# Optimization experiments

Measured on AMD Instinct MI355X. Metric: run time of the kernel, lower is better.

Reference implementation:

```python
import jax, jax.numpy as jnp
import numpy as np

NUM_GRAPHS = 256  # static batch size (= batch_indices.max()+1 by construction)
EMBED = 32
HIDDEN = 256
DEPTH = 10


def setup_inputs() -> dict:
    key = jax.random.key(0)
    ks = jax.random.split(key, 16)
    N, M = 8192, 16384
    atom_features = jax.random.randint(ks[0], (N,), 0, 200, dtype=jnp.int32)
    bond_features = jax.random.randint(ks[1], (M,), 0, 10, dtype=jnp.int32)
    adjacency_matrix = jax.random.randint(ks[2], (N, N), 0, 2, dtype=jnp.int32)
    batch_indices = jnp.sort(jax.random.randint(ks[3], (N,), 0, NUM_GRAPHS, dtype=jnp.int32))
    s = 0.05
    atom_emb_table = jax.random.normal(ks[4], (200, EMBED), jnp.float32) * s
    bond_emb_table = jax.random.normal(ks[5], (10, EMBED), jnp.float32) * s
    msg_W = jax.random.normal(ks[6], (DEPTH, HIDDEN, 2 * EMBED), jnp.float32) * s
    msg_b = jax.random.normal(ks[7], (DEPTH, HIDDEN), jnp.float32) * s
    gru_Wih = jax.random.normal(ks[8], (DEPTH, 3 * EMBED, HIDDEN), jnp.float32) * s
    gru_Whh = jax.random.normal(ks[9], (DEPTH, 3 * EMBED, EMBED), jnp.float32) * s
    gru_bih = jax.random.normal(ks[10], (DEPTH, 3 * EMBED), jnp.float32) * s
    gru_bhh = jax.random.normal(ks[11], (DEPTH, 3 * EMBED), jnp.float32) * s
    pool_W = jax.random.normal(ks[12], (HIDDEN, EMBED), jnp.float32) * s
    pool_b = jax.random.normal(ks[13], (HIDDEN,), jnp.float32) * s
    return dict(atom_features=atom_features, bond_features=bond_features,
                adjacency_matrix=adjacency_matrix, batch_indices=batch_indices,
                atom_emb_table=atom_emb_table, bond_emb_table=bond_emb_table,
                msg_W=msg_W, msg_b=msg_b, gru_Wih=gru_Wih, gru_Whh=gru_Whh,
                gru_bih=gru_bih, gru_bhh=gru_bhh, pool_W=pool_W, pool_b=pool_b)


def _gru_step(x, h, Wih, Whh, bih, bhh):
    # single-step torch-style GRU cell: x [N,HIDDEN], h [N,EMBED]
    gi = x @ Wih.T + bih                      # [N, 3E]
    gh = h @ Whh.T + bhh                      # [N, 3E]
    i_r, i_z, i_n = jnp.split(gi, 3, axis=-1)
    h_r, h_z, h_n = jnp.split(gh, 3, axis=-1)
    r = jax.nn.sigmoid(i_r + h_r)
    z = jax.nn.sigmoid(i_z + h_z)
    n = jnp.tanh(i_n + r * h_n)
    return (1.0 - z) * n + z * h


def reference(atom_features, bond_features, adjacency_matrix, batch_indices,
              atom_emb_table, bond_emb_table, msg_W, msg_b,
              gru_Wih, gru_Whh, gru_bih, gru_bhh, pool_W, pool_b):
    h = atom_emb_table[atom_features]                      # [N, E]
    A = (adjacency_matrix != 0).astype(h.dtype)            # [N, N]
    deg = A.sum(axis=-1, keepdims=True)                    # [N, 1]
    inv_deg = 1.0 / jnp.maximum(deg, 1.0)
    has_nei = deg > 0
    for d in range(DEPTH):
        # mean over neighbors of Linear(concat(self, nei)) == affine in (self, mean_nei)
        nei_mean = (A @ h) * inv_deg                       # [N, E]
        W_self = msg_W[d][:, :EMBED]                       # [H, E]
        W_nei = msg_W[d][:, EMBED:]                        # [H, E]
        msg = h @ W_self.T + nei_mean @ W_nei.T + msg_b[d]  # [N, H]
        msg = jnp.where(has_nei, msg, 0.0)                 # zero message if no neighbors
        h = _gru_step(msg, h, gru_Wih[d], gru_Whh[d], gru_bih[d], gru_bhh[d])
        # dropout is identity in eval mode
    # segment-mean pooling over graphs (zeros for empty graphs)
    sums = jax.ops.segment_sum(h, batch_indices, num_segments=NUM_GRAPHS)      # [B, E]
    counts = jax.ops.segment_sum(jnp.ones((h.shape[0],), h.dtype), batch_indices,
                                 num_segments=NUM_GRAPHS)[:, None]             # [B, 1]
    graph_mean = jnp.where(counts > 0, sums / jnp.maximum(counts, 1.0), 0.0)
    graph_embeddings = graph_mean @ pool_W.T + pool_b                          # [B, H]
    bond_embeddings = bond_emb_table[bond_features]                            # [M, E]
    return h, bond_embeddings, graph_embeddings
```

## Files before the change

### kernel.cpp

```cpp
#include <hip/hip_runtime.h>
#include <stdint.h>

#define N_ATOMS 8192
#define EMBED   32
#define DEPTHN  10

typedef short bf16x8 __attribute__((ext_vector_type(8)));
typedef float f32x4  __attribute__((ext_vector_type(4)));

__device__ __forceinline__ unsigned short f2bf(float f){
    unsigned u = __builtin_bit_cast(unsigned, f);
    u = u + 0x7FFFu + ((u >> 16) & 1u);
    return (unsigned short)(u >> 16);
}

__global__ __launch_bounds__(256) void k_preA(const int* __restrict__ A,
                                              unsigned long long* __restrict__ mask,
                                              int row0)
{
    const int i = row0 + blockIdx.x;
    const int t = threadIdx.x, w = t >> 6, l = t & 63;
    const int* row = A + (size_t)i * N_ATOMS;
    __shared__ unsigned long long lm[128];
    #pragma unroll
    for (int k = 0; k < 32; ++k){
        int j = k*256 + t;
        unsigned long long m = __ballot(row[j] != 0);
        if (l == 0) lm[k*4 + w] = m;
    }
    __syncthreads();
    if (t < 128) mask[(size_t)i*128 + t] = lm[t];
}

__global__ __launch_bounds__(256) void k_pre2(
    const int* __restrict__ A, unsigned* __restrict__ mP,
    float* __restrict__ deg, float* __restrict__ invdeg,
    const int* __restrict__ af, const float* __restrict__ atom_emb,
    const float* __restrict__ msgW, const float* __restrict__ msgb,
    const float* __restrict__ Wih, const float* __restrict__ bih,
    float* __restrict__ hA, unsigned short* __restrict__ hP,
    float* __restrict__ Wc, float* __restrict__ bc,
    const int* __restrict__ bfeat, const float* __restrict__ bondf,
    float* __restrict__ out1)
{
    const int t = threadIdx.x;
    __shared__ unsigned lm[256];
    __shared__ int red[4];
    if (blockIdx.x < 8192){
        const int blk = blockIdx.x;
        const int grp = (blk >> 7)*8 + (blk & 7);
        const int n   = (blk >> 3) & 15;
        const int i   = grp*16 + n;
        const int w = t >> 6, l = t & 63;
        const int* row = A + (size_t)i * N_ATOMS;
        #pragma unroll
        for (int k = 0; k < 32; ++k){
            int j = k*256 + t;
            unsigned long long m = __ballot(row[j] != 0);
            if (l == 0){
                lm[(k*4 + w)*2]     = (unsigned)m;
                lm[(k*4 + w)*2 + 1] = (unsigned)(m >> 32);
            }
        }
        __syncthreads();
        int cnt = __popc(lm[t]);
        #pragma unroll
        for (int off = 32; off >= 1; off >>= 1) cnt += __shfl_down(cnt, off, 64);
        if (l == 0) red[w] = cnt;
        __syncthreads();
        if (t == 0){
            int s = red[0] + red[1] + red[2] + red[3];
            deg[i] = (float)s;
            invdeg[i] = 1.f / fmaxf((float)s, 1.f);
        }
        mP[(size_t)grp*4096 + t*16 + n] = lm[t];
    } else {
        const int blk = blockIdx.x - 8192;
        if (blk < 1024){
            int idx = blk*256 + t;
            int i = idx >> 5, e = idx & 31;
            float v = atom_emb[af[i]*EMBED + e];
            hA[idx] = v;
            int g = i >> 5, qd = (i >> 3) & 3, j8 = i & 7;
            hP[(size_t)((g*2 + (e>>4))*64 + qd*16 + (e&15))*8 + j8] = f2bf(v);
        } else if (blk < 1264){
            int o = (blk-1024)*256 + t;
            int d = o / 6144, r = o % 6144, g = r >> 6, e = r & 63;
            const float* wi = Wih  + (size_t)(d*96 + g)*256;
            const float* mw = msgW + (size_t)d*256*64 + e;
            float acc = 0.f;
            for (int hh = 0; hh < 256; ++hh) acc += wi[hh] * mw[hh*64];
            Wc[o] = acc;
        } else if (blk < 1268){
            int o = (blk-1264)*256 + t;
            if (o < 960){
                int d = o / 96;
                const float* wi = Wih + (size_t)o*256;
                const float* mb = msgb + d*256;
                float acc = 0.f;
                for (int hh = 0; hh < 256; ++hh) acc += wi[hh] * mb[hh];
                bc[o] = acc + bih[o];
            }
        } else {
            int idx = (blk-1268)*256 + t;
            out1[idx] = bondf[bfeat[idx >> 5]*EMBED + (idx & 31)];
        }
    }
}

__global__ __launch_bounds__(256) void k_prep(
    const unsigned* __restrict__ maskRM, unsigned* __restrict__ mP,
    float* __restrict__ deg, float* __restrict__ invdeg,
    const int* __restrict__ af, const float* __restrict__ atom_emb,
    const float* __restrict__ msgW, const float* __restrict__ msgb,
    const float* __restrict__ Wih, const float* __restrict__ bih,
    float* __restrict__ hA, unsigned short* __restrict__ hP,
    float* __restrict__ Wc, float* __restrict__ bc,
    const int* __restrict__ bfeat, const float* __restrict__ bondf,
    float* __restrict__ out1)
{
    const int t = threadIdx.x;
    if (blockIdx.x < 512){
        const int grp = blockIdx.x;
        __shared__ unsigned lm[16*260];
        __shared__ int red[256];
        #pragma unroll
        for (int s = 0; s < 16; ++s)
            lm[s*260 + t] = maskRM[(size_t)grp*4096 + s*256 + t];
        __syncthreads();
        {
            int r = t >> 4, seg = t & 15, cnt = 0;
            #pragma unroll
            for (int k = 0; k < 16; ++k) cnt += __popc(lm[r*260 + seg*16 + k]);
            red[t] = cnt; __syncthreads();
            if (t < 16){
                int s = 0;
                #pragma unroll
                for (int k = 0; k < 16; ++k) s += red[t*16 + k];
                deg[grp*16 + t] = (float)s;
                invdeg[grp*16 + t] = 1.f / fmaxf((float)s, 1.f);
            }
        }
        unsigned* out = mP + (size_t)grp*4096;
        #pragma unroll
        for (int s = 0; s < 16; ++s){
            int W = s*256 + t;
            out[W] = lm[(W & 15)*260 + (W >> 4)];
        }
    } else {
        const int blk = blockIdx.x - 512;
        if (blk < 1024){
            int idx = blk*256 + t;
            int i = idx >> 5, e = idx & 31;
            float v = atom_emb[af[i]*EMBED + e];
            hA[idx] = v;
            int g = i >> 5, qd = (i >> 3) & 3, j8 = i & 7;
            hP[(size_t)((g*2 + (e>>4))*64 + qd*16 + (e&15))*8 + j8] = f2bf(v);
        } else if (blk < 1264){
            int o = (blk-1024)*256 + t;
            int d = o / 6144, r = o % 6144, g = r >> 6, e = r & 63;
            const float* wi = Wih  + (size_t)(d*96 + g)*256;
            const float* mw = msgW + (size_t)d*256*64 + e;
            float acc = 0.f;
            for (int hh = 0; hh < 256; ++hh) acc += wi[hh] * mw[hh*64];
            Wc[o] = acc;
        } else if (blk < 1268){
            int o = (blk-1264)*256 + t;
            if (o < 960){
                int d = o / 96;
                const float* wi = Wih + (size_t)o*256;
                const float* mb = msgb + d*256;
                float acc = 0.f;
                for (int hh = 0; hh < 256; ++hh) acc += wi[hh] * mb[hh];
                bc[o] = acc + bih[o];
            }
        } else {
            int idx = (blk-1268)*256 + t;
            out1[idx] = bondf[bfeat[idx >> 5]*EMBED + (idx & 31)];
        }
    }
}

__global__ __launch_bounds__(512) void k_depth(
    const unsigned short* __restrict__ hPin,
    const unsigned* __restrict__ mP,
    const float* __restrict__ hin, float* __restrict__ hout,
    const float* __restrict__ invdeg, const float* __restrict__ deg,
    const float* __restrict__ Wc, const float* __restrict__ bc,
    const float* __restrict__ bihf, const float* __restrict__ bhhf,
    const float* __restrict__ Whhf,
    unsigned short* __restrict__ hPout, float* __restrict__ out0, int last)
{
    __shared__ uint2 lut[16];
    __shared__ float part[8][32][33];
    __shared__ float xs[32][68];
    const int t = threadIdx.x, blk = blockIdx.x;
    if (t < 16){
        unsigned lo = ((t & 1) ? 0x3F80u : 0u) | ((t & 2) ? 0x3F800000u : 0u);
        unsigned hi = ((t & 4) ? 0x3F80u : 0u) | ((t & 8) ? 0x3F800000u : 0u);
        lut[t] = make_uint2(lo, hi);
    }
    __syncthreads();
    {
        const int q = t >> 6, lane = t & 63;
        const int n = lane & 15, quad = lane >> 4;
        const int rt0 = blk*2;
        f32x4 a00 = {0.f,0.f,0.f,0.f};
        f32x4 a01 = {0.f,0.f,0.f,0.f};
        f32x4 a10 = {0.f,0.f,0.f,0.f};
        f32x4 a11 = {0.f,0.f,0.f,0.f};
        const unsigned* m0 = mP + (size_t)rt0*4096 + n;
        const unsigned* m1 = m0 + 4096;
        #pragma unroll 4
        for (int kk = 0; kk < 32; ++kk){
            const int g = q*32 + kk;
            union { uint4 u; bf16x8 v; } b0, b1;
            b0.u = *(const uint4*)&hPin[(size_t)((g*2+0)*64 + lane)*8];
            b1.u = *(const uint4*)&hPin[(size_t)((g*2+1)*64 + lane)*8];
            unsigned by0 = (m0[g*16] >> (quad*8)) & 0xFFu;
            unsigned by1 = (m1[g*16] >> (quad*8)) & 0xFFu;
            union { uint2 dd[2]; bf16x8 v; } af0, af1;
            af0.dd[0] = lut[by0 & 15u];
            af0.dd[1] = lut[by0 >> 4];
            af1.dd[0] = lut[by1 & 15u];
            af1.dd[1] = lut[by1 >> 4];
            a00 = __builtin_amdgcn_mfma_f32_16x16x32_bf16(af0.v, b0.v, a00, 0, 0, 0);
            a01 = __builtin_amdgcn_mfma_f32_16x16x32_bf16(af0.v, b1.v, a01, 0, 0, 0);
            a10 = __builtin_amdgcn_mfma_f32_16x16x32_bf16(af1.v, b0.v, a10, 0, 0, 0);
            a11 = __builtin_amdgcn_mfma_f32_16x16x32_bf16(af1.v, b1.v, a11, 0, 0, 0);
        }
        #pragma unroll
        for (int r = 0; r < 4; ++r){
            int rl = quad*4 + r;
            part[q][rl][n]       = a00[r];
            part[q][rl][16+n]    = a01[r];
            part[q][16+rl][n]    = a10[r];
            part[q][16+rl][16+n] = a11[r];
        }
    }
    __syncthreads();
    {
        #pragma unroll
        for (int ii = 0; ii < 2; ++ii){
            int i = ii*512 + t;
            int a = i >> 5, e = i & 31;
            float s = 0.f;
            #pragma unroll
            for (int q = 0; q < 8; ++q) s += part[q][a][e];
            xs[a][32+e] = s;
            xs[a][e] = hin[(size_t)blk*1024 + i];
        }
    }
    __syncthreads();
    {
        const int a = t & 15, pw = t >> 4;
        const int al = a + (pw & 16);
        const int p  = pw & 15;
        const int atom = blk*32 + al;
        const float idg = invdeg[atom];
        const bool nz = deg[atom] > 0.f;
        float x[64];
        #pragma unroll
        for (int r = 0; r < 16; ++r){
            float4 v = *(const float4*)&xs[al][r*4];
            x[r*4+0]=v.x; x[r*4+1]=v.y; x[r*4+2]=v.z; x[r*4+3]=v.w;
        }
        #pragma unroll
        for (int e = 32; e < 64; ++e) x[e] *= idg;
        const int gg = atom >> 5, qd = (atom >> 3) & 3, j8 = atom & 7;
        #pragma unroll
        for (int jj = 0; jj < 2; ++jj){
            const int j = p*2 + jj;
            const float* wr = Wc + j*64;
            const float* wz = Wc + (32+j)*64;
            const float* wn = Wc + (64+j)*64;
            float gr=0.f, gz=0.f, gn=0.f;
            #pragma unroll
            for (int e = 0; e < 64; ++e){ gr += wr[e]*x[e]; gz += wz[e]*x[e]; gn += wn[e]*x[e]; }
            if (nz){ gr += bc[j]; gz += bc[32+j]; gn += bc[64+j]; }
            else   { gr  = bihf[j]; gz = bihf[32+j]; gn = bihf[64+j]; }
            const float* vr = Whhf + j*32;
            const float* vz = Whhf + (32+j)*32;
            const float* vn = Whhf + (64+j)*32;
            float hr=bhhf[j], hz=bhhf[32+j], hn=bhhf[64+j];
            #pragma unroll
            for (int e = 0; e < 32; ++e){ hr += vr[e]*x[e]; hz += vz[e]*x[e]; hn += vn[e]*x[e]; }
            float rg = 1.f/(1.f + expf(-(gr+hr)));
            float zg = 1.f/(1.f + expf(-(gz+hz)));
            float ng = tanhf(gn + rg*hn);
            float hnew = (1.f - zg)*ng + zg*x[j];
            hout[(size_t)atom*EMBED + j] = hnew;
            hPout[(size_t)((gg*2 + (j>>4))*64 + qd*16 + (j&15))*8 + j8] = f2bf(hnew);
            if (last) out0[(size_t)atom*EMBED + j] = hnew;
        }
    }
}

__global__ __launch_bounds__(256) void k_pool(
    const float* __restrict__ h, const int* __restrict__ batch,
    const float* __restrict__ poolW, const float* __restrict__ poolb,
    float* __restrict__ out2)
{
    const int b = blockIdx.x, t = threadIdx.x;
    int lo, hi;
    { int l = 0, r = N_ATOMS; while (l < r){ int m = (l+r)>>1; if (batch[m] < b)   l = m+1; else r = m; } lo = l; }
    { int l = 0, r = N_ATOMS; while (l < r){ int m = (l+r)>>1; if (batch[m] < b+1) l = m+1; else r = m; } hi = l; }
    const int cnt = hi - lo;
    __shared__ float ps[8][32];
    __shared__ float mean[32];
    const int e = t & 31, g = t >> 5;
    float acc = 0.f;
    for (int a = lo + g; a < hi; a += 8) acc += h[(size_t)a*EMBED + e];
    ps[g][e] = acc; __syncthreads();
    if (t < 32){
        float s = 0.f;
        #pragma unroll
        for (int gg = 0; gg < 8; ++gg) s += ps[gg][t];
        mean[t] = (cnt > 0) ? s / (float)cnt : 0.f;
    }
    __syncthreads();
    float emb = poolb[t];
    #pragma unroll
    for (int ee = 0; ee < 32; ++ee) emb += mean[ee] * poolW[t*32 + ee];
    out2[b*256 + t] = emb;
}

extern "C" void kernel_launch(void* const* d_in, const int* in_sizes, int n_in,
                              void* d_out, int out_size, void* d_ws, size_t ws_size,
                              hipStream_t stream)
{
    (void)in_sizes; (void)n_in; (void)out_size;
    const int* af   = (const int*)d_in[0];
    const int* bfe  = (const int*)d_in[1];
    const int* A    = (const int*)d_in[2];
    const int* bidx = (const int*)d_in[3];
    const float* atom_emb = (const float*)d_in[4];
    const float* bond_emb = (const float*)d_in[5];
    const float* msgW  = (const float*)d_in[6];
    const float* msgb  = (const float*)d_in[7];
    const float* Wih   = (const float*)d_in[8];
    const float* Whh   = (const float*)d_in[9];
    const float* bih   = (const float*)d_in[10];
    const float* bhh   = (const float*)d_in[11];
    const float* poolW = (const float*)d_in[12];
    const float* poolb = (const float*)d_in[13];

    float* out0 = (float*)d_out;
    float* out1 = out0 + 262144;
    float* out2 = out1 + 524288;

    float* deg    = out2;
    float* invdeg = out2 + 8192;

    unsigned*       mP;
    float*          hA; float* hB; float* Wc; float* bc;
    unsigned short* hP0; unsigned short* hP1;
    const int wsok = (ws_size >= (size_t)33554432) ? 1 : 0;
    if (wsok){
        char* W = (char*)d_ws;
        mP      = (unsigned*)(W + 8388608);
        hP0     = (unsigned short*)(W + 16777216);
        hA      = (float*)(W + 17825792);
        hB      = (float*)(W + 18874368);
        Wc      = (float*)(W + 19922944);
        bc      = (float*)(W + 20185088);
        hP1     = (unsigned short*)(W + 20971520);
        k_pre2<<<dim3(11508), dim3(256), 0, stream>>>(A, mP, deg, invdeg,
            af, atom_emb, msgW, msgb, Wih, bih, hA, hP0, Wc, bc,
            bfe, bond_emb, out1);
    } else {
        unsigned long long* maskRM;
        char* Ab = (char*)d_in[2];
        hA      = (float*)(Ab + 0);
        hB      = (float*)(Ab + 1048576);
        hP0     = (unsigned short*)(Ab + 2097152);
        Wc      = (float*)(Ab + 2621440);
        bc      = (float*)(Ab + 2867200);
        hP1     = (unsigned short*)(Ab + 4194304);
        mP      = (unsigned*)(Ab + 13631488);
        maskRM  = (unsigned long long*)(Ab + 260046848);
        k_preA<<<dim3(1),    dim3(256), 0, stream>>>(A, maskRM, 8191);
        k_preA<<<dim3(7),    dim3(256), 0, stream>>>(A, maskRM, 8184);
        k_preA<<<dim3(248),  dim3(256), 0, stream>>>(A, maskRM, 7936);
        k_preA<<<dim3(7936), dim3(256), 0, stream>>>(A, maskRM, 0);
        k_prep<<<dim3(3828), dim3(256), 0, stream>>>((const unsigned*)maskRM, mP,
            deg, invdeg, af, atom_emb, msgW, msgb, Wih, bih, hA, hP0, Wc, bc,
            bfe, bond_emb, out1);
    }

    float* hin = hA; float* hout = hB;
    unsigned short* hPi = hP0; unsigned short* hPo = hP1;
    for (int d = 0; d < DEPTHN; ++d){
        k_depth<<<dim3(256), dim3(512), 0, stream>>>(hPi, mP, hin, hout,
            invdeg, deg, Wc + d*6144, bc + d*96, bih + d*96, bhh + d*96,
            Whh + d*3072, hPo, out0, (d == DEPTHN-1) ? 1 : 0);
        float* tf = hin; hin = hout; hout = tf;
        unsigned short* tp = hPi; hPi = hPo; hPo = tp;
    }
    k_pool<<<dim3(256), dim3(256), 0, stream>>>(hin, bidx, poolW, poolb, out2);
}
```

Baseline: 666.5 us.

## Process 64 atoms per depth block to reuse h tiles across four row tiles

Each k_depth block now covers 64 atoms (four 16-row mask tiles) instead of 32, so every loaded bf16 h fragment feeds eight MFMAs rather than four. This halves global reads of h per depth step. The partial-sum reduction now runs in two phases through a smaller shared buffer to fit LDS, and the GRU stage gives each thread four output columns. The grid shrinks to 128 blocks, which lowers parallelism on a GPU with many CUs, and k_pre2 block ordering is swapped so the mask-packing blocks come after the other preprocessing blocks.

Measured after the change: 800.6 us. +20.1%, slower.

```diff
diff --git a/kernel.cpp b/kernel.cpp
--- a/kernel.cpp
+++ b/kernel.cpp
@@ -46,8 +46,8 @@
     const int t = threadIdx.x;
     __shared__ unsigned lm[256];
     __shared__ int red[4];
-    if (blockIdx.x < 8192){
-        const int blk = blockIdx.x;
+    if (blockIdx.x >= 3316){
+        const int blk = blockIdx.x - 3316;
         const int grp = (blk >> 7)*8 + (blk & 7);
         const int n   = (blk >> 3) & 15;
         const int i   = grp*16 + n;
@@ -75,7 +75,7 @@
         }
         mP[(size_t)grp*4096 + t*16 + n] = lm[t];
     } else {
-        const int blk = blockIdx.x - 8192;
+        const int blk = blockIdx.x;
         if (blk < 1024){
             int idx = blk*256 + t;
             int i = idx >> 5, e = idx & 31;
@@ -192,8 +192,8 @@
     unsigned short* __restrict__ hPout, float* __restrict__ out0, int last)
 {
     __shared__ uint2 lut[16];
-    __shared__ float part[8][32][33];
-    __shared__ float xs[32][68];
+    __shared__ float part[4][64][33];
+    __shared__ float xs[64][68];
     const int t = threadIdx.x, blk = blockIdx.x;
     if (t < 16){
         unsigned lo = ((t & 1) ? 0x3F80u : 0u) | ((t & 2) ? 0x3F800000u : 0u);
@@ -201,62 +201,77 @@
         lut[t] = make_uint2(lo, hi);
     }
     __syncthreads();
+    const int q = t >> 6, lane = t & 63;
+    const int n = lane & 15, quad = lane >> 4;
     {
-        const int q = t >> 6, lane = t & 63;
-        const int n = lane & 15, quad = lane >> 4;
-        const int rt0 = blk*2;
-        f32x4 a00 = {0.f,0.f,0.f,0.f};
-        f32x4 a01 = {0.f,0.f,0.f,0.f};
-        f32x4 a10 = {0.f,0.f,0.f,0.f};
-        f32x4 a11 = {0.f,0.f,0.f,0.f};
-        const unsigned* m0 = mP + (size_t)rt0*4096 + n;
-        const unsigned* m1 = m0 + 4096;
+        const int rt0 = blk*4;
+        f32x4 acc[4][2];
+        #pragma unroll
+        for (int r = 0; r < 4; ++r){
+            acc[r][0] = (f32x4){0.f,0.f,0.f,0.f};
+            acc[r][1] = (f32x4){0.f,0.f,0.f,0.f};
+        }
+        const unsigned* mb_ = mP + (size_t)rt0*4096 + n;
         #pragma unroll 4
         for (int kk = 0; kk < 32; ++kk){
             const int g = q*32 + kk;
             union { uint4 u; bf16x8 v; } b0, b1;
             b0.u = *(const uint4*)&hPin[(size_t)((g*2+0)*64 + lane)*8];
             b1.u = *(const uint4*)&hPin[(size_t)((g*2+1)*64 + lane)*8];
-            unsigned by0 = (m0[g*16] >> (quad*8)) & 0xFFu;
-            unsigned by1 = (m1[g*16] >> (quad*8)) & 0xFFu;
-            union { uint2 dd[2]; bf16x8 v; } af0, af1;
-            af0.dd[0] = lut[by0 & 15u];
-            af0.dd[1] = lut[by0 >> 4];
-            af1.dd[0] = lut[by1 & 15u];
-            af1.dd[1] = lut[by1 >> 4];
-            a00 = __builtin_amdgcn_mfma_f32_16x16x32_bf16(af0.v, b0.v, a00, 0, 0, 0);
-            a01 = __builtin_amdgcn_mfma_f32_16x16x32_bf16(af0.v, b1.v, a01, 0, 0, 0);
-            a10 = __builtin_amdgcn_mfma_f32_16x16x32_bf16(af1.v, b0.v, a10, 0, 0, 0);
-            a11 = __builtin_amdgcn_mfma_f32_16x16x32_bf16(af1.v, b1.v, a11, 0, 0, 0);
-        }
-        #pragma unroll
-        for (int r = 0; r < 4; ++r){
-            int rl = quad*4 + r;
-            part[q][rl][n]       = a00[r];
-            part[q][rl][16+n]    = a01[r];
-            part[q][16+rl][n]    = a10[r];
-            part[q][16+rl][16+n] = a11[r];
+            #pragma unroll
+            for (int rt = 0; rt < 4; ++rt){
+                unsigned by = (mb_[(size_t)rt*4096 + g*16] >> (quad*8)) & 0xFFu;
+                union { uint2 dd[2]; bf16x8 v; } afx;
+                afx.dd[0] = lut[by & 15u];
+                afx.dd[1] = lut[by >> 4];
+                acc[rt][0] = __builtin_amdgcn_mfma_f32_16x16x32_bf16(afx.v, b0.v, acc[rt][0], 0, 0, 0);
+                acc[rt][1] = __builtin_amdgcn_mfma_f32_16x16x32_bf16(afx.v, b1.v, acc[rt][1], 0, 0, 0);
+            }
+        }
+        if (q < 4){
+            #pragma unroll
+            for (int rt = 0; rt < 4; ++rt)
+                #pragma unroll
+                for (int r = 0; r < 4; ++r){
+                    int rl = rt*16 + quad*4 + r;
+                    part[q][rl][n]      = acc[rt][0][r];
+                    part[q][rl][16+n]   = acc[rt][1][r];
+                }
+        }
+        __syncthreads();
+        float s[4];
+        #pragma unroll
+        for (int k = 0; k < 4; ++k){
+            int i = k*512 + t;
+            int a2 = i >> 5, e = i & 31;
+            s[k] = part[0][a2][e] + part[1][a2][e] + part[2][a2][e] + part[3][a2][e];
+            xs[a2][e] = hin[(size_t)blk*2048 + i];
+        }
+        __syncthreads();
+        if (q >= 4){
+            #pragma unroll
+            for (int rt = 0; rt < 4; ++rt)
+                #pragma unroll
+                for (int r = 0; r < 4; ++r){
+                    int rl = rt*16 + quad*4 + r;
+                    part[q-4][rl][n]    = acc[rt][0][r];
+                    part[q-4][rl][16+n] = acc[rt][1][r];
+                }
+        }
+        __syncthreads();
+        #pragma unroll
+        for (int k = 0; k < 4; ++k){
+            int i = k*512 + t;
+            int a2 = i >> 5, e = i & 31;
+            s[k] += part[0][a2][e] + part[1][a2][e] + part[2][a2][e] + part[3][a2][e];
+            xs[a2][32+e] = s[k];
         }
     }
     __syncthreads();
     {
-        #pragma unroll
-        for (int ii = 0; ii < 2; ++ii){
-            int i = ii*512 + t;
-            int a = i >> 5, e = i & 31;
-            float s = 0.f;
-            #pragma unroll
-            for (int q = 0; q < 8; ++q) s += part[q][a][e];
-            xs[a][32+e] = s;
-            xs[a][e] = hin[(size_t)blk*1024 + i];
-        }
-    }
-    __syncthreads();
-    {
-        const int a = t & 15, pw = t >> 4;
-        const int al = a + (pw & 16);
-        const int p  = pw & 15;
-        const int atom = blk*32 + al;
+        const int al = t & 63;
+        const int p  = t >> 6;
+        const int atom = blk*64 + al;
         const float idg = invdeg[atom];
         const bool nz = deg[atom] > 0.f;
         float x[64];
@@ -269,8 +284,8 @@
         for (int e = 32; e < 64; ++e) x[e] *= idg;
         const int gg = atom >> 5, qd = (atom >> 3) & 3, j8 = atom & 7;
         #pragma unroll
-        for (int jj = 0; jj < 2; ++jj){
-            const int j = p*2 + jj;
+        for (int jj = 0; jj < 4; ++jj){
+            const int j = p*4 + jj;
             const float* wr = Wc + j*64;
             const float* wz = Wc + (32+j)*64;
             const float* wn = Wc + (64+j)*64;
@@ -391,7 +406,7 @@
     float* hin = hA; float* hout = hB;
     unsigned short* hPi = hP0; unsigned short* hPo = hP1;
     for (int d = 0; d < DEPTHN; ++d){
-        k_depth<<<dim3(256), dim3(512), 0, stream>>>(hPi, mP, hin, hout,
+        k_depth<<<dim3(128), dim3(512), 0, stream>>>(hPi, mP, hin, hout,
             invdeg, deg, Wc + d*6144, bc + d*96, bih + d*96, bhh + d*96,
             Whh + d*3072, hPo, out0, (d == DEPTHN-1) ? 1 : 0);
         float* tf = hin; hin = hout; hout = tf;
```
